# Performance work log

Hardware: AMD Instinct MI355X
Metric: run time of the kernel (lower is better)

Reference implementation:

```python
import jax, jax.numpy as jnp
import numpy as np

D, B, L, E, H, F = 6, 4, 2048, 1024, 16, 4096
DH = E // H
DECAY = 16.0
CSCALE = 1.0
EPS = 1e-5


def _ln(x, w, b):
    m = jnp.mean(x, axis=-1, keepdims=True)
    v = jnp.mean(jnp.square(x - m), axis=-1, keepdims=True)
    return (x - m) * jax.lax.rsqrt(v + EPS) * w + b


def setup_inputs() -> dict:
    key = jax.random.key(0)
    ks = jax.random.split(key, 10)
    s = 0.02
    f32 = jnp.float32
    return {
        "x": jax.random.normal(ks[0], (B, L, E), f32),
        "Wq": jax.random.normal(ks[1], (D, E, E), f32) * s,
        "Wk": jax.random.normal(ks[2], (D, E, E), f32) * s,
        "bq": jnp.zeros((D, E), f32),
        "bk": jnp.zeros((D, E), f32),
        "ln1_w": jnp.ones((D, E), f32), "ln1_b": jnp.zeros((D, E), f32),
        "ln2_w": jnp.ones((D, E), f32), "ln2_b": jnp.zeros((D, E), f32),
        "ln3_w": jnp.ones((D, E), f32), "ln3_b": jnp.zeros((D, E), f32),
        "W1": jax.random.normal(ks[3], (D, F, E), f32) * s,
        "b1": jnp.zeros((D, F), f32),
        "W2": jax.random.normal(ks[4], (D, E, F), f32) * s,
        "b2": jnp.zeros((D, E), f32),
    }


def reference(x, Wq, Wk, bq, bk, ln1_w, ln1_b, ln2_w, ln2_b, ln3_w, ln3_b, W1, b1, W2, b2):
    seq = x.shape[1]
    pos = jnp.arange(seq)
    # exponential relative-position bias exp(-|i-j|/decay), shared by all layers
    rel = jnp.exp(-jnp.abs(pos[:, None] - pos[None, :]).astype(x.dtype) / DECAY)
    inv_sqrt_d = 1.0 / np.sqrt(DH)

    def layer(h, p):
        (wq, wk, bq_, bk_, l1w, l1b, l2w, l2b, l3w, l3b, w1, b1_, w2, b2_) = p
        bh, sl, _ = h.shape
        q = (h @ wq.T + bq_).reshape(bh, sl, H, DH)
        k = (h @ wk.T + bk_).reshape(bh, sl, H, DH)
        scores = jnp.einsum('blhd,bmhd->bhlm', q, k) * inv_sqrt_d
        # torch MHA need_weights=True averages softmax weights over heads
        w_avg = jax.nn.softmax(scores, axis=-1).mean(axis=1)  # [B,L,L]
        new_w = jax.nn.softmax(CSCALE * w_avg + rel[None], axis=-1)
        sa = jnp.einsum('blm,bme->ble', new_w, h)  # value = raw residual stream
        h1 = _ln(h + sa, l1w, l1b)
        h2 = _ln(h1, l2w, l2b)  # Noop cross-attn block (LayerNorm scale-invariant)
        ff = jax.nn.relu(h2 @ w1.T + b1_) @ w2.T + b2_
        return _ln(h2 + ff, l3w, l3b), None

    out, _ = jax.lax.scan(layer, x, (Wq, Wk, bq, bk, ln1_w, ln1_b, ln2_w, ln2_b,
                                     ln3_w, ln3_b, W1, b1, W2, b2))
    return out
```

## Files before the change

### kernel.cpp

```cpp
#include <hip/hip_runtime.h>

#define D_ 6
#define B_ 4
#define L_ 2048
#define E_ 1024
#define H_ 16
#define F_ 4096
#define BL_ (B_ * L_)
#define QKS 2048
#define EPS_ 1e-5f
#define EXPSC 0.18033688011112042f
#define LOG2E 1.4426950408889634f
#define LOG2E_H (LOG2E / 16.0f)

typedef __bf16 bf16x8 __attribute__((ext_vector_type(8)));
typedef __bf16 bf16x4 __attribute__((ext_vector_type(4)));
typedef float f32x4 __attribute__((ext_vector_type(4)));

__device__ __forceinline__ float fexp2(float x) {
  return __builtin_amdgcn_exp2f(x);
}

__device__ __forceinline__ void gload_lds16(const void* g, void* l) {
  __builtin_amdgcn_global_load_lds(
      (const __attribute__((address_space(1))) void*)g,
      (__attribute__((address_space(3))) void*)l, 16, 0, 0);
}

__device__ __forceinline__ void stage_tile64(__bf16* ldsb,
                                             const __bf16* gbase, long ldg,
                                             int tid) {
#pragma unroll
  for (int j = 0; j < 2; ++j) {
    int unit = j * 256 + tid;
    int row = unit >> 3, cu = unit & 7;
    const __bf16* src = gbase + (long)row * ldg + ((cu ^ (row & 7)) << 3);
    gload_lds16(src, ldsb + (long)((j * 256 + (tid & ~63)) << 3));
  }
}

#define RD_FRAG(ldsb, r_, kk) \
  (*(const bf16x8*)&(ldsb)[((r_) * 8 + (((kk) * 4 + l4) ^ ((r_) & 7))) * 8])

#define LDA_SUB(P, MH)                                                        \
  _Pragma("unroll") for (int mi = 0; mi < 4; ++mi)                            \
  _Pragma("unroll") for (int kk = 0; kk < 2; ++kk) {                          \
    int r_ = wr + (MH) * 64 + mi * 16 + l15;                                  \
    int cu_ = kk * 4 + l4;                                                    \
    aF[mi][kk] = *(const bf16x8*)&lds[P][0][(r_ * 8 + (cu_ ^ (r_ & 7))) * 8]; \
  }

#define LDB_SUB(P, BF, NH)                                                    \
  _Pragma("unroll") for (int ni = 0; ni < 2; ++ni)                            \
  _Pragma("unroll") for (int kk = 0; kk < 2; ++kk) {                          \
    int r_ = wc + (NH) * 32 + ni * 16 + l15;                                  \
    int cu_ = kk * 4 + l4;                                                    \
    BF[ni][kk] = *(const bf16x8*)&lds[P][1][(r_ * 8 + (cu_ ^ (r_ & 7))) * 8]; \
  }

#define MFMA_Q(AF, BF, MH, NH)                                                \
  _Pragma("unroll") for (int mi = 0; mi < 4; ++mi)                            \
  _Pragma("unroll") for (int ni = 0; ni < 2; ++ni)                            \
  _Pragma("unroll") for (int kk = 0; kk < 2; ++kk)                            \
    acc[(MH) * 4 + mi][(NH) * 2 + ni] =                                       \
        __builtin_amdgcn_mfma_f32_16x16x32_bf16(                              \
            AF[mi][kk], BF[ni][kk], acc[(MH) * 4 + mi][(NH) * 2 + ni], 0, 0, 0);

#define PHASE_PRE()                                                           \
  __builtin_amdgcn_s_barrier();                                               \
  asm volatile("s_waitcnt lgkmcnt(0)" ::: "memory");                          \
  __builtin_amdgcn_sched_barrier(0);                                          \
  __builtin_amdgcn_s_setprio(1)

#define PHASE_POST()                                                          \
  __builtin_amdgcn_s_setprio(0);                                              \
  __builtin_amdgcn_sched_barrier(0);                                          \
  __builtin_amdgcn_s_barrier()

#define STAGE_A(BUFI, HF, K0)                                                 \
  do {                                                                        \
    gload_lds16(sA[HF][0] + (K0),                                             \
                &lds[BUFI][0][((HF) * 1024 + wave * 64) * 8]);                \
    gload_lds16(sA[HF][1] + (K0),                                             \
                &lds[BUFI][0][((HF) * 1024 + 512 + wave * 64) * 8]);          \
  } while (0)

#define STAGE_B(BUFI, HF, K0)                                                 \
  do {                                                                        \
    gload_lds16(sB[HF][0] + (K0),                                             \
                &lds[BUFI][1][((HF) * 1024 + wave * 64) * 8]);                \
    gload_lds16(sB[HF][1] + (K0),                                             \
                &lds[BUFI][1][((HF) * 1024 + 512 + wave * 64) * 8]);          \
  } while (0)

template <int EPI>
__global__ __launch_bounds__(512, 2) void gemm8p(
    const __bf16* __restrict__ A, const __bf16* __restrict__ Bm,
    __bf16* __restrict__ Cb, const float* __restrict__ bias, int M, int N,
    int K, int lda, int ldb, int zk, long strA, long strB, long strC,
    long strCk) {
  __shared__ __bf16 lds[2][2][256 * 64];
  const int tid = threadIdx.x;
  const int wave = tid >> 6, lane = tid & 63;
  const int l15 = lane & 15, l4 = lane >> 4;
  const int z = blockIdx.y;
  const int kc = (zk == 2) ? (z & 1) : 0;
  const int bat = (zk == 2) ? (z >> 1) : z;
  const __bf16* Ab = A + (long)bat * strA + (long)kc * K;
  const __bf16* Bb = Bm + (long)bat * strB + (long)kc * K;
  const long coff = (long)bat * strC + (long)kc * strCk;

  const int nbx = N >> 8;
  const int nwg = (M >> 8) * nbx;
  const int orig = blockIdx.x;
  const int qq = nwg >> 3, rr = nwg & 7;
  const int xcd = orig & 7, lid = orig >> 3;
  const int wg = (xcd < rr ? xcd * (qq + 1) : rr * (qq + 1) + (xcd - rr) * qq) + lid;
  const int row0 = (wg / nbx) * 256, col0 = (wg % nbx) * 256;
  const int wr = (wave >> 2) * 128;
  const int wc = (wave & 3) * 64;

  const int rsel = tid >> 3;
  const int swz = ((lane & 7) ^ (rsel & 7)) << 3;
  const __bf16* sA[2][2];
  const __bf16* sB[2][2];
#pragma unroll
  for (int hf = 0; hf < 2; ++hf)
#pragma unroll
    for (int j = 0; j < 2; ++j) {
      sA[hf][j] = Ab + (long)(row0 + hf * 128 + j * 64 + rsel) * lda + swz;
      sB[hf][j] = Bb + (long)(col0 + hf * 128 + j * 64 + rsel) * ldb + swz;
    }

  const int NT = K >> 6;
  STAGE_A(0, 0, 0);
  STAGE_A(0, 1, 0);
  STAGE_B(0, 0, 0);
  STAGE_B(0, 1, 0);
  STAGE_A(1, 0, 64);
  STAGE_B(1, 0, 64);
  STAGE_A(1, 1, 64);
  asm volatile("s_waitcnt vmcnt(6)" ::: "memory");
  __builtin_amdgcn_s_barrier();

  f32x4 acc[8][4];
#pragma unroll
  for (int i = 0; i < 8; ++i)
#pragma unroll
    for (int j = 0; j < 4; ++j) acc[i][j] = (f32x4){0.f, 0.f, 0.f, 0.f};
  bf16x8 aF[4][2], b0F[2][2], b1F[2][2];

  for (int t = 0; t < NT; ++t) {
    const int p = t & 1;
    const int kA = (t + 1 < NT ? t + 1 : NT - 1) << 6;
    const int kB = (t + 2 < NT ? t + 2 : NT - 1) << 6;
    LDA_SUB(p, 0);
    LDB_SUB(p, b0F, 0);
    STAGE_B(p ^ 1, 1, kA);
    PHASE_PRE();
    MFMA_Q(aF, b0F, 0, 0);
    PHASE_POST();
    LDB_SUB(p, b1F, 1);
    PHASE_PRE();
    MFMA_Q(aF, b1F, 0, 1);
    PHASE_POST();
    LDA_SUB(p, 1);
    STAGE_B(p, 0, kB);
    PHASE_PRE();
    MFMA_Q(aF, b0F, 1, 0);
    PHASE_POST();
    STAGE_A(p, 0, kB);
    STAGE_A(p, 1, kB);
    __builtin_amdgcn_s_barrier();
    __builtin_amdgcn_sched_barrier(0);
    __builtin_amdgcn_s_setprio(1);
    MFMA_Q(aF, b1F, 1, 1);
    __builtin_amdgcn_s_setprio(0);
    __builtin_amdgcn_sched_barrier(0);
    asm volatile("s_waitcnt vmcnt(6)" ::: "memory");
    __builtin_amdgcn_s_barrier();
  }
  asm volatile("s_waitcnt vmcnt(0)" ::: "memory");

#pragma unroll
  for (int i = 0; i < 8; ++i) {
    int row = row0 + wr + (i >> 2) * 64 + (i & 3) * 16 + l4 * 4;
#pragma unroll
    for (int j = 0; j < 4; ++j) {
      int col = col0 + wc + (j >> 1) * 32 + (j & 1) * 16 + l15;
      float bval = 0.f;
      if constexpr (EPI == 1 || EPI == 2) bval = bias[col];
#pragma unroll
      for (int r = 0; r < 4; ++r) {
        long crow = row + r;
        float v = acc[i][j][r];
        if constexpr (EPI == 1 || EPI == 2) v += bval;
        if constexpr (EPI == 2) v = fmaxf(v, 0.f);
        Cb[coff + crow * N + col] = (__bf16)v;
      }
    }
  }
}

__global__ __launch_bounds__(256, 4) void attn_stats_kernel(
    const __bf16* __restrict__ qk, float* __restrict__ sinv) {
  __shared__ __bf16 sQ[64 * 64];
  __shared__ __bf16 sK[2][64 * 64];
  const int tid = threadIdx.x, wave = tid >> 6, lane = tid & 63;
  const int l15 = lane & 15, l4 = lane >> 4;
  const int l0 = blockIdx.x * 64, h = blockIdx.y, b = blockIdx.z;
  const __bf16* Qb = qk + ((long)(b * L_ + l0)) * QKS + h * 64;
  const __bf16* Kb = qk + ((long)b * L_) * QKS + 1024 + h * 64;

  stage_tile64(sQ, Qb, QKS, tid);
  stage_tile64(sK[0], Kb, QKS, tid);
  asm volatile("s_waitcnt vmcnt(0)" ::: "memory");
  __builtin_amdgcn_s_barrier();

  const int rA = wave * 16 + l15;
  const bf16x8 aF0 = RD_FRAG(sQ, rA, 0);
  const bf16x8 aF1 = RD_FRAG(sQ, rA, 1);

  float msum[4] = {0.f, 0.f, 0.f, 0.f};
  int p = 0;
  for (int m0 = 0; m0 < 32; ++m0) {
    const int mn = (m0 + 1 < 32) ? m0 + 1 : 31;
    stage_tile64(sK[p ^ 1], Kb + (long)mn * 64 * QKS, QKS, tid);
    asm volatile("s_waitcnt vmcnt(2)" ::: "memory");
    __builtin_amdgcn_s_barrier();
#pragma unroll
    for (int ni = 0; ni < 4; ++ni) {
      const int rB = ni * 16 + l15;
      bf16x8 b0 = RD_FRAG(sK[p], rB, 0);
      bf16x8 b1 = RD_FRAG(sK[p], rB, 1);
      f32x4 s = (f32x4){0.f, 0.f, 0.f, 0.f};
      s = __builtin_amdgcn_mfma_f32_16x16x32_bf16(aF0, b0, s, 0, 0, 0);
      s = __builtin_amdgcn_mfma_f32_16x16x32_bf16(aF1, b1, s, 0, 0, 0);
#pragma unroll
      for (int r = 0; r < 4; ++r) msum[r] += fexp2(s[r]);
    }
    asm volatile("" ::: "memory");
    __builtin_amdgcn_s_barrier();
    p ^= 1;
  }
#pragma unroll
  for (int r = 0; r < 4; ++r) {
    float s = msum[r];
    for (int d = 1; d < 16; d <<= 1) s += __shfl_xor(s, d, 64);
    msum[r] = s;
  }
  if (l15 == 0) {
    long idx = ((long)(b * H_ + h)) * L_ + l0 + wave * 16 + l4 * 4;
    f32x4 o = {1.0f / msum[0], 1.0f / msum[1], 1.0f / msum[2], 1.0f / msum[3]};
    *(f32x4*)&sinv[idx] = o;
  }
}

__global__ __launch_bounds__(256, 4) void attn_probs_kernel(
    const __bf16* __restrict__ qk, const float* __restrict__ sinv,
    const float* __restrict__ relTab, __bf16* __restrict__ P,
    float* __restrict__ rowsumT) {
  __shared__ __bf16 sT[2][2][64 * 64];
  const int tid = threadIdx.x, wave = tid >> 6, lane = tid & 63;
  const int l15 = lane & 15, l4 = lane >> 4;
  const int m0 = blockIdx.x * 64, l0 = blockIdx.y * 64, b = blockIdx.z;
  const __bf16* Qb = qk + ((long)(b * L_ + l0)) * QKS;
  const __bf16* Kb = qk + ((long)(b * L_ + m0)) * QKS + 1024;

  stage_tile64(sT[0][0], Qb, QKS, tid);
  stage_tile64(sT[0][1], Kb, QKS, tid);

  float wacc[4][4];
#pragma unroll
  for (int i = 0; i < 4; ++i)
#pragma unroll
    for (int j = 0; j < 4; ++j) wacc[i][j] = 0.f;

  const int rA = wave * 16 + l15;
  const int row0 = l0 + wave * 16 + l4 * 4;
  int p = 0;
  for (int h = 0; h < H_; ++h) {
    const int hn = (h + 1 < H_) ? h + 1 : H_ - 1;
    stage_tile64(sT[p ^ 1][0], Qb + hn * 64, QKS, tid);
    stage_tile64(sT[p ^ 1][1], Kb + hn * 64, QKS, tid);
    f32x4 iv = *(const f32x4*)&sinv[((long)(b * H_ + h)) * L_ + row0];
    asm volatile("s_waitcnt vmcnt(4)" ::: "memory");
    __builtin_amdgcn_s_barrier();
    bf16x8 aF0 = RD_FRAG(sT[p][0], rA, 0);
    bf16x8 aF1 = RD_FRAG(sT[p][0], rA, 1);
#pragma unroll
    for (int ni = 0; ni < 4; ++ni) {
      const int rB = ni * 16 + l15;
      bf16x8 b0 = RD_FRAG(sT[p][1], rB, 0);
      bf16x8 b1 = RD_FRAG(sT[p][1], rB, 1);
      f32x4 s = (f32x4){0.f, 0.f, 0.f, 0.f};
      s = __builtin_amdgcn_mfma_f32_16x16x32_bf16(aF0, b0, s, 0, 0, 0);
      s = __builtin_amdgcn_mfma_f32_16x16x32_bf16(aF1, b1, s, 0, 0, 0);
#pragma unroll
      for (int r = 0; r < 4; ++r) wacc[ni][r] += fexp2(s[r]) * iv[r];
    }
    asm volatile("" ::: "memory");
    __builtin_amdgcn_s_barrier();
    p ^= 1;
  }
  float rowpart[4] = {0.f, 0.f, 0.f, 0.f};
#pragma unroll
  for (int ni = 0; ni < 4; ++ni) {
#pragma unroll
    for (int r = 0; r < 4; ++r) {
      int row = row0 + r;
      int col = m0 + ni * 16 + l15;
      float relL = relTab[row - col + 2048];
      float pv = fexp2(fmaf(wacc[ni][r], LOG2E_H, relL));
      P[((long)b * L_ + row) * L_ + col] = (__bf16)pv;
      rowpart[r] += pv;
    }
  }
#pragma unroll
  for (int r = 0; r < 4; ++r) {
    float s = rowpart[r];
    s += __shfl_xor(s, 1, 16);
    s += __shfl_xor(s, 2, 16);
    s += __shfl_xor(s, 4, 16);
    s += __shfl_xor(s, 8, 16);
    if (l15 == 0)
      rowsumT[((long)b * L_ + row0 + r) * 32 + (m0 >> 6)] = s;
  }
}

__device__ __forceinline__ void wave_reduce2(float& a, float& b) {
#pragma unroll
  for (int d = 1; d < 64; d <<= 1) {
    a += __shfl_xor(a, d, 64);
    b += __shfl_xor(b, d, 64);
  }
}

__global__ __launch_bounds__(256, 4) void ln12_kernel(
    const float* __restrict__ hin, const __bf16* __restrict__ p0,
    const __bf16* __restrict__ p1, const float* __restrict__ rowsumT,
    const float* __restrict__ w1, const float* __restrict__ b1,
    const float* __restrict__ w2, const float* __restrict__ b2,
    float* __restrict__ h2f, __bf16* __restrict__ h2b) {
  __shared__ float sh[9];
  const int tid = threadIdx.x;
  const long row = blockIdx.x;
  const long base = row * E_ + tid * 4;
  if (tid < 32) {
    float s = rowsumT[row * 32 + tid];
#pragma unroll
    for (int d = 1; d < 32; d <<= 1) s += __shfl_xor(s, d, 32);
    if (tid == 0) sh[8] = s;
  }
  f32x4 hv = *(const f32x4*)&hin[base];
  bf16x4 p0v = *(const bf16x4*)&p0[base];
  bf16x4 p1v = *(const bf16x4*)&p1[base];
  __syncthreads();
  const float rinv = 1.0f / sh[8];
  float y[4];
  float s1 = 0.f, s2 = 0.f;
#pragma unroll
  for (int j = 0; j < 4; ++j) {
    y[j] = hv[j] + rinv * ((float)p0v[j] + (float)p1v[j]);
    s1 += y[j];
    s2 += y[j] * y[j];
  }
  wave_reduce2(s1, s2);
  if ((tid & 63) == 0) { sh[(tid >> 6) * 2] = s1; sh[(tid >> 6) * 2 + 1] = s2; }
  __syncthreads();
  s1 = sh[0] + sh[2] + sh[4] + sh[6];
  s2 = sh[1] + sh[3] + sh[5] + sh[7];
  float mean = s1 * (1.f / E_);
  float var = s2 * (1.f / E_) - mean * mean;
  float rs = rsqrtf(var + EPS_);
  f32x4 wv = *(const f32x4*)&w1[tid * 4];
  f32x4 bv = *(const f32x4*)&b1[tid * 4];
  float h1[4];
  s1 = 0.f; s2 = 0.f;
#pragma unroll
  for (int j = 0; j < 4; ++j) {
    h1[j] = (y[j] - mean) * rs * wv[j] + bv[j];
    s1 += h1[j];
    s2 += h1[j] * h1[j];
  }
  __syncthreads();
  wave_reduce2(s1, s2);
  if ((tid & 63) == 0) { sh[(tid >> 6) * 2] = s1; sh[(tid >> 6) * 2 + 1] = s2; }
  __syncthreads();
  s1 = sh[0] + sh[2] + sh[4] + sh[6];
  s2 = sh[1] + sh[3] + sh[5] + sh[7];
  mean = s1 * (1.f / E_);
  var = s2 * (1.f / E_) - mean * mean;
  rs = rsqrtf(var + EPS_);
  wv = *(const f32x4*)&w2[tid * 4];
  bv = *(const f32x4*)&b2[tid * 4];
  f32x4 o;
  bf16x4 ob;
#pragma unroll
  for (int j = 0; j < 4; ++j) {
    float v = (h1[j] - mean) * rs * wv[j] + bv[j];
    o[j] = v;
    ob[j] = (__bf16)v;
  }
  *(f32x4*)&h2f[base] = o;
  *(bf16x4*)&h2b[base] = ob;
}

__global__ __launch_bounds__(256, 4) void ln3_kernel(
    const float* __restrict__ h2f, const __bf16* __restrict__ p0,
    const __bf16* __restrict__ p1, const float* __restrict__ bias2,
    const float* __restrict__ w3, const float* __restrict__ b3,
    float* __restrict__ outf, __bf16* __restrict__ outb) {
  __shared__ float sh[8];
  const int tid = threadIdx.x;
  const long row = blockIdx.x;
  const long base = row * E_ + tid * 4;
  f32x4 hv = *(const f32x4*)&h2f[base];
  bf16x4 p0v = *(const bf16x4*)&p0[base];
  bf16x4 p1v = *(const bf16x4*)&p1[base];
  f32x4 b2v = *(const f32x4*)&bias2[tid * 4];
  float y[4];
  float s1 = 0.f, s2 = 0.f;
#pragma unroll
  for (int j = 0; j < 4; ++j) {
    y[j] = hv[j] + (float)p0v[j] + (float)p1v[j] + b2v[j];
    s1 += y[j];
    s2 += y[j] * y[j];
  }
  wave_reduce2(s1, s2);
  if ((tid & 63) == 0) { sh[(tid >> 6) * 2] = s1; sh[(tid >> 6) * 2 + 1] = s2; }
  __syncthreads();
  s1 = sh[0] + sh[2] + sh[4] + sh[6];
  s2 = sh[1] + sh[3] + sh[5] + sh[7];
  float mean = s1 * (1.f / E_);
  float var = s2 * (1.f / E_) - mean * mean;
  float rs = rsqrtf(var + EPS_);
  f32x4 wv = *(const f32x4*)&w3[tid * 4];
  f32x4 bv = *(const f32x4*)&b3[tid * 4];
  f32x4 o;
  bf16x4 ob;
#pragma unroll
  for (int j = 0; j < 4; ++j) {
    float v = (y[j] - mean) * rs * wv[j] + bv[j];
    o[j] = v;
    ob[j] = (__bf16)v;
  }
  *(f32x4*)&outf[base] = o;
  *(bf16x4*)&outb[base] = ob;
}

__global__ __launch_bounds__(256, 4) void transpose_kernel(
    const __bf16* __restrict__ X, __bf16* __restrict__ XT) {
  __shared__ __bf16 t[64 * 66];
  const int l0 = blockIdx.x * 64, e0 = blockIdx.y * 64, b = blockIdx.z;
  const int tid = threadIdx.x;
#pragma unroll
  for (int r = 0; r < 2; ++r) {
    int c = tid + 256 * r;
    int rw = c >> 3, c8 = (c & 7) * 8;
    *(bf16x8*)&t[rw * 66 + c8] =
        *(const bf16x8*)&X[((long)(b * L_) + l0 + rw) * E_ + e0 + c8];
  }
  __syncthreads();
#pragma unroll
  for (int r = 0; r < 2; ++r) {
    int c = tid + 256 * r;
    int er = c >> 3, l8 = (c & 7) * 8;
    bf16x8 v;
#pragma unroll
    for (int j = 0; j < 8; ++j) v[j] = t[(l8 + j) * 66 + er];
    *(bf16x8*)&XT[((long)(b * E_) + e0 + er) * L_ + l0 + l8] = v;
  }
}

__global__ __launch_bounds__(256, 4) void f32_to_bf16_kernel(
    const float* __restrict__ x, __bf16* __restrict__ y) {
  long i = ((long)blockIdx.x * 256 + threadIdx.x) * 4;
  f32x4 v = *(const f32x4*)&x[i];
  bf16x4 o;
#pragma unroll
  for (int j = 0; j < 4; ++j) o[j] = (__bf16)v[j];
  *(bf16x4*)&y[i] = o;
}

__global__ __launch_bounds__(256, 4) void build_wqk_kernel(
    const float* __restrict__ Wq, const float* __restrict__ Wk,
    __bf16* __restrict__ out) {
  long i = ((long)blockIdx.x * 256 + threadIdx.x) * 4;
  long d = i >> 21;
  long rem = i & ((1L << 21) - 1);
  long row = rem >> 10, col = rem & 1023;
  const bool isQ = (row < 1024);
  const float* src = isQ ? &Wq[(d << 20) + (row << 10) + col]
                         : &Wk[(d << 20) + ((row - 1024) << 10) + col];
  const float sc = isQ ? EXPSC : 1.0f;
  f32x4 v = *(const f32x4*)src;
  bf16x4 o;
#pragma unroll
  for (int j = 0; j < 4; ++j) o[j] = (__bf16)(v[j] * sc);
  *(bf16x4*)&out[i] = o;
}

__global__ __launch_bounds__(256, 4) void build_bqk_kernel(
    const float* __restrict__ bq, const float* __restrict__ bk,
    float* __restrict__ out) {
  int i = blockIdx.x * 256 + threadIdx.x;
  int d = i >> 11, c = i & 2047;
  out[i] = (c < 1024) ? bq[d * 1024 + c] * EXPSC : bk[d * 1024 + c - 1024];
}

__global__ __launch_bounds__(256, 4) void build_rel_kernel(
    float* __restrict__ relTab) {
  int i = blockIdx.x * 256 + threadIdx.x;
  relTab[i] = __expf(-fabsf((float)(i - 2048)) * (1.0f / 16.0f)) * LOG2E;
}

extern "C" void kernel_launch(void* const* d_in, const int* in_sizes, int n_in,
                              void* d_out, int out_size, void* d_ws,
                              size_t ws_size, hipStream_t stream) {
  const float* x = (const float*)d_in[0];
  const float* Wq = (const float*)d_in[1];
  const float* Wk = (const float*)d_in[2];
  const float* bq = (const float*)d_in[3];
  const float* bk = (const float*)d_in[4];
  const float* l1w = (const float*)d_in[5];
  const float* l1b = (const float*)d_in[6];
  const float* l2w = (const float*)d_in[7];
  const float* l2b = (const float*)d_in[8];
  const float* l3w = (const float*)d_in[9];
  const float* l3b = (const float*)d_in[10];
  const float* W1 = (const float*)d_in[11];
  const float* b1 = (const float*)d_in[12];
  const float* W2 = (const float*)d_in[13];
  const float* b2 = (const float*)d_in[14];

  char* p = (char*)d_ws;
  auto take = [&](size_t bytes) -> char* {
    char* r = p;
    p += (bytes + 255) & ~(size_t)255;
    return r;
  };
  __bf16* wqk_bf = (__bf16*)take((size_t)D_ * 2048 * 1024 * 2);
  __bf16* w1_bf = (__bf16*)take((size_t)D_ * F_ * E_ * 2);
  __bf16* w2_bf = (__bf16*)take((size_t)D_ * E_ * F_ * 2);
  __bf16* h_bf = (__bf16*)take((size_t)BL_ * E_ * 2);
  __bf16* hT = (__bf16*)take((size_t)BL_ * E_ * 2);
  __bf16* qk_bf = (__bf16*)take((size_t)BL_ * QKS * 2);
  __bf16* Pbuf = (__bf16*)take((size_t)B_ * L_ * L_ * 2);
  __bf16* ffmid = qk_bf;
  float* bqk = (float*)take((size_t)D_ * 2048 * 4);
  float* relTab = (float*)take((size_t)4096 * 4);
  float* sinv = (float*)take((size_t)B_ * H_ * L_ * 4);
  float* rowsumT = (float*)take((size_t)BL_ * 32 * 4);
  __bf16* partB = (__bf16*)take((size_t)2 * BL_ * E_ * 2);
  __bf16* part0 = partB;
  __bf16* part1 = partB + (size_t)BL_ * E_;
  float* hbuf = (float*)take((size_t)BL_ * E_ * 4);

  build_wqk_kernel<<<D_ * 2048 * 1024 / 1024, 256, 0, stream>>>(Wq, Wk, wqk_bf);
  build_bqk_kernel<<<D_ * 2048 / 256, 256, 0, stream>>>(bq, bk, bqk);
  build_rel_kernel<<<16, 256, 0, stream>>>(relTab);
  f32_to_bf16_kernel<<<D_ * F_ * E_ / 1024, 256, 0, stream>>>(W1, w1_bf);
  f32_to_bf16_kernel<<<D_ * E_ * F_ / 1024, 256, 0, stream>>>(W2, w2_bf);
  f32_to_bf16_kernel<<<BL_ * E_ / 1024, 256, 0, stream>>>(x, h_bf);
  transpose_kernel<<<dim3(L_ / 64, E_ / 64, B_), 256, 0, stream>>>(h_bf, hT);

  const float* h_in = x;
  for (int d = 0; d < D_; ++d) {
    gemm8p<1><<<dim3(256, 1), 512, 0, stream>>>(
        h_bf, wqk_bf + (size_t)d * 2048 * 1024, qk_bf, bqk + d * 2048, BL_,
        2048, E_, E_, E_, 1, 0, 0, 0, 0);
    attn_stats_kernel<<<dim3(L_ / 64, H_, B_), 256, 0, stream>>>(qk_bf, sinv);
    attn_probs_kernel<<<dim3(L_ / 64, L_ / 64, B_), 256, 0, stream>>>(
        qk_bf, sinv, relTab, Pbuf, rowsumT);
    gemm8p<0><<<dim3(32, 8), 512, 0, stream>>>(
        Pbuf, hT, partB, nullptr, L_, E_, L_ / 2, L_, L_, 2, (long)L_ * L_,
        (long)E_ * L_, (long)L_ * E_, (long)BL_ * E_);
    ln12_kernel<<<BL_, 256, 0, stream>>>(h_in, part0, part1, rowsumT,
                                         l1w + d * E_, l1b + d * E_,
                                         l2w + d * E_, l2b + d * E_, hbuf,
                                         h_bf);
    gemm8p<2><<<dim3(512, 1), 512, 0, stream>>>(
        h_bf, w1_bf + (size_t)d * F_ * E_, ffmid, b1 + d * F_, BL_, F_, E_,
        E_, E_, 1, 0, 0, 0, 0);
    gemm8p<0><<<dim3(128, 2), 512, 0, stream>>>(
        ffmid, w2_bf + (size_t)d * E_ * F_, partB, nullptr, BL_, E_, F_ / 2,
        F_, F_, 2, 0, 0, 0, (long)BL_ * E_);
    float* outp = (d == D_ - 1) ? (float*)d_out : hbuf;
    ln3_kernel<<<BL_, 256, 0, stream>>>(hbuf, part0, part1, b2 + d * E_,
                                        l3w + d * E_, l3b + d * E_, outp,
                                        h_bf);
    if (d < D_ - 1) {
      transpose_kernel<<<dim3(L_ / 64, E_ / 64, B_), 256, 0, stream>>>(h_bf, hT);
      h_in = hbuf;
    }
  }
}
```

Before: 2.325 ms.

## Enlarge attention stats/probs tiles to 128 rows with 512-thread blocks

The attention statistics kernel now processes 128 query rows per block with 8 waves, so each staged K tile is reused by twice as many rows. The probabilities kernel moves from 64x64 to 128x128 output tiles with 8 waves, each computing 32x64, which cuts redundant global/LDS loads of Q and K per head. The cost is more LDS and registers per block, lower occupancy (launch bounds 2) and fewer blocks in the grid.

```diff
diff --git a/kernel.cpp b/kernel.cpp
--- a/kernel.cpp
+++ b/kernel.cpp
@@ -36,6 +36,26 @@
     int row = unit >> 3, cu = unit & 7;
     const __bf16* src = gbase + (long)row * ldg + ((cu ^ (row & 7)) << 3);
     gload_lds16(src, ldsb + (long)((j * 256 + (tid & ~63)) << 3));
+  }
+}
+
+__device__ __forceinline__ void stage_tile64_512(__bf16* ldsb,
+                                                 const __bf16* gbase, long ldg,
+                                                 int tid) {
+  int row = tid >> 3, cu = tid & 7;
+  const __bf16* src = gbase + (long)row * ldg + ((cu ^ (row & 7)) << 3);
+  gload_lds16(src, ldsb + (long)((tid & ~63) << 3));
+}
+
+__device__ __forceinline__ void stage_tile128_512(__bf16* ldsb,
+                                                  const __bf16* gbase,
+                                                  long ldg, int tid) {
+#pragma unroll
+  for (int j = 0; j < 2; ++j) {
+    int unit = j * 512 + tid;
+    int row = unit >> 3, cu = unit & 7;
+    const __bf16* src = gbase + (long)row * ldg + ((cu ^ (row & 7)) << 3);
+    gload_lds16(src, ldsb + (long)((j * 512 + (tid & ~63)) << 3));
   }
 }
 
@@ -202,18 +222,18 @@
   }
 }
 
-__global__ __launch_bounds__(256, 4) void attn_stats_kernel(
+__global__ __launch_bounds__(512, 4) void attn_stats_kernel(
     const __bf16* __restrict__ qk, float* __restrict__ sinv) {
-  __shared__ __bf16 sQ[64 * 64];
+  __shared__ __bf16 sQ[128 * 64];
   __shared__ __bf16 sK[2][64 * 64];
   const int tid = threadIdx.x, wave = tid >> 6, lane = tid & 63;
   const int l15 = lane & 15, l4 = lane >> 4;
-  const int l0 = blockIdx.x * 64, h = blockIdx.y, b = blockIdx.z;
+  const int l0 = blockIdx.x * 128, h = blockIdx.y, b = blockIdx.z;
   const __bf16* Qb = qk + ((long)(b * L_ + l0)) * QKS + h * 64;
   const __bf16* Kb = qk + ((long)b * L_) * QKS + 1024 + h * 64;
 
-  stage_tile64(sQ, Qb, QKS, tid);
-  stage_tile64(sK[0], Kb, QKS, tid);
+  stage_tile128_512(sQ, Qb, QKS, tid);
+  stage_tile64_512(sK[0], Kb, QKS, tid);
   asm volatile("s_waitcnt vmcnt(0)" ::: "memory");
   __builtin_amdgcn_s_barrier();
 
@@ -225,8 +245,8 @@
   int p = 0;
   for (int m0 = 0; m0 < 32; ++m0) {
     const int mn = (m0 + 1 < 32) ? m0 + 1 : 31;
-    stage_tile64(sK[p ^ 1], Kb + (long)mn * 64 * QKS, QKS, tid);
-    asm volatile("s_waitcnt vmcnt(2)" ::: "memory");
+    stage_tile64_512(sK[p ^ 1], Kb + (long)mn * 64 * QKS, QKS, tid);
+    asm volatile("s_waitcnt vmcnt(1)" ::: "memory");
     __builtin_amdgcn_s_barrier();
 #pragma unroll
     for (int ni = 0; ni < 4; ++ni) {
@@ -256,75 +276,94 @@
   }
 }
 
-__global__ __launch_bounds__(256, 4) void attn_probs_kernel(
+__global__ __launch_bounds__(512, 2) void attn_probs_kernel(
     const __bf16* __restrict__ qk, const float* __restrict__ sinv,
     const float* __restrict__ relTab, __bf16* __restrict__ P,
     float* __restrict__ rowsumT) {
-  __shared__ __bf16 sT[2][2][64 * 64];
+  __shared__ __bf16 sQ[2][128 * 64];
+  __shared__ __bf16 sKl[2][128 * 64];
   const int tid = threadIdx.x, wave = tid >> 6, lane = tid & 63;
   const int l15 = lane & 15, l4 = lane >> 4;
-  const int m0 = blockIdx.x * 64, l0 = blockIdx.y * 64, b = blockIdx.z;
+  const int m0 = blockIdx.x * 128, l0 = blockIdx.y * 128, b = blockIdx.z;
+  const int wr2 = wave & 3, wc2 = wave >> 2;
   const __bf16* Qb = qk + ((long)(b * L_ + l0)) * QKS;
   const __bf16* Kb = qk + ((long)(b * L_ + m0)) * QKS + 1024;
 
-  stage_tile64(sT[0][0], Qb, QKS, tid);
-  stage_tile64(sT[0][1], Kb, QKS, tid);
-
-  float wacc[4][4];
+  stage_tile128_512(sQ[0], Qb, QKS, tid);
+  stage_tile128_512(sKl[0], Kb, QKS, tid);
+
+  float wacc[4][8];
 #pragma unroll
   for (int i = 0; i < 4; ++i)
 #pragma unroll
-    for (int j = 0; j < 4; ++j) wacc[i][j] = 0.f;
-
-  const int rA = wave * 16 + l15;
-  const int row0 = l0 + wave * 16 + l4 * 4;
+    for (int j = 0; j < 8; ++j) wacc[i][j] = 0.f;
+
+  const int rA0 = wr2 * 32 + l15;
+  const int rowbase = l0 + wr2 * 32 + l4 * 4;
   int p = 0;
   for (int h = 0; h < H_; ++h) {
     const int hn = (h + 1 < H_) ? h + 1 : H_ - 1;
-    stage_tile64(sT[p ^ 1][0], Qb + hn * 64, QKS, tid);
-    stage_tile64(sT[p ^ 1][1], Kb + hn * 64, QKS, tid);
-    f32x4 iv = *(const f32x4*)&sinv[((long)(b * H_ + h)) * L_ + row0];
+    stage_tile128_512(sQ[p ^ 1], Qb + hn * 64, QKS, tid);
+    stage_tile128_512(sKl[p ^ 1], Kb + hn * 64, QKS, tid);
+    const float* svh = &sinv[((long)(b * H_ + h)) * L_];
+    f32x4 iv0 = *(const f32x4*)&svh[rowbase];
+    f32x4 iv1 = *(const f32x4*)&svh[rowbase + 16];
     asm volatile("s_waitcnt vmcnt(4)" ::: "memory");
     __builtin_amdgcn_s_barrier();
-    bf16x8 aF0 = RD_FRAG(sT[p][0], rA, 0);
-    bf16x8 aF1 = RD_FRAG(sT[p][0], rA, 1);
+    bf16x8 aF[2][2];
+    aF[0][0] = RD_FRAG(sQ[p], rA0, 0);
+    aF[0][1] = RD_FRAG(sQ[p], rA0, 1);
+    aF[1][0] = RD_FRAG(sQ[p], rA0 + 16, 0);
+    aF[1][1] = RD_FRAG(sQ[p], rA0 + 16, 1);
 #pragma unroll
     for (int ni = 0; ni < 4; ++ni) {
-      const int rB = ni * 16 + l15;
-      bf16x8 b0 = RD_FRAG(sT[p][1], rB, 0);
-      bf16x8 b1 = RD_FRAG(sT[p][1], rB, 1);
-      f32x4 s = (f32x4){0.f, 0.f, 0.f, 0.f};
-      s = __builtin_amdgcn_mfma_f32_16x16x32_bf16(aF0, b0, s, 0, 0, 0);
-      s = __builtin_amdgcn_mfma_f32_16x16x32_bf16(aF1, b1, s, 0, 0, 0);
-#pragma unroll
-      for (int r = 0; r < 4; ++r) wacc[ni][r] += fexp2(s[r]) * iv[r];
+      const int rB = wc2 * 64 + ni * 16 + l15;
+      bf16x8 b0 = RD_FRAG(sKl[p], rB, 0);
+      bf16x8 b1 = RD_FRAG(sKl[p], rB, 1);
+#pragma unroll
+      for (int fi = 0; fi < 2; ++fi) {
+        f32x4 s = (f32x4){0.f, 0.f, 0.f, 0.f};
+        s = __builtin_amdgcn_mfma_f32_16x16x32_bf16(aF[fi][0], b0, s, 0, 0, 0);
+        s = __builtin_amdgcn_mfma_f32_16x16x32_bf16(aF[fi][1], b1, s, 0, 0, 0);
+#pragma unroll
+        for (int r = 0; r < 4; ++r)
+          wacc[ni][fi * 4 + r] += fexp2(s[r]) * (fi ? iv1[r] : iv0[r]);
+      }
     }
     asm volatile("" ::: "memory");
     __builtin_amdgcn_s_barrier();
     p ^= 1;
   }
-  float rowpart[4] = {0.f, 0.f, 0.f, 0.f};
+  float rowpart[2][4] = {{0.f, 0.f, 0.f, 0.f}, {0.f, 0.f, 0.f, 0.f}};
 #pragma unroll
   for (int ni = 0; ni < 4; ++ni) {
 #pragma unroll
+    for (int fi = 0; fi < 2; ++fi) {
+#pragma unroll
+      for (int r = 0; r < 4; ++r) {
+        int row = rowbase + fi * 16 + r;
+        int col = m0 + wc2 * 64 + ni * 16 + l15;
+        float relL = relTab[row - col + 2048];
+        float pv = fexp2(fmaf(wacc[ni][fi * 4 + r], LOG2E_H, relL));
+        P[((long)b * L_ + row) * L_ + col] = (__bf16)pv;
+        rowpart[fi][r] += pv;
+      }
+    }
+  }
+#pragma unroll
+  for (int fi = 0; fi < 2; ++fi) {
+#pragma unroll
     for (int r = 0; r < 4; ++r) {
-      int row = row0 + r;
-      int col = m0 + ni * 16 + l15;
-      float relL = relTab[row - col + 2048];
-      float pv = fexp2(fmaf(wacc[ni][r], LOG2E_H, relL));
-      P[((long)b * L_ + row) * L_ + col] = (__bf16)pv;
-      rowpart[r] += pv;
+      float s = rowpart[fi][r];
+      s += __shfl_xor(s, 1, 16);
+      s += __shfl_xor(s, 2, 16);
+      s += __shfl_xor(s, 4, 16);
+      s += __shfl_xor(s, 8, 16);
+      if (l15 == 0) {
+        int row = rowbase + fi * 16 + r;
+        rowsumT[((long)b * L_ + row) * 32 + (m0 >> 6) + wc2] = s;
+      }
     }
-  }
-#pragma unroll
-  for (int r = 0; r < 4; ++r) {
-    float s = rowpart[r];
-    s += __shfl_xor(s, 1, 16);
-    s += __shfl_xor(s, 2, 16);
-    s += __shfl_xor(s, 4, 16);
-    s += __shfl_xor(s, 8, 16);
-    if (l15 == 0)
-      rowsumT[((long)b * L_ + row0 + r) * 32 + (m0 >> 6)] = s;
   }
 }
 
@@ -570,8 +609,8 @@
     gemm8p<1><<<dim3(256, 1), 512, 0, stream>>>(
         h_bf, wqk_bf + (size_t)d * 2048 * 1024, qk_bf, bqk + d * 2048, BL_,
         2048, E_, E_, E_, 1, 0, 0, 0, 0);
-    attn_stats_kernel<<<dim3(L_ / 64, H_, B_), 256, 0, stream>>>(qk_bf, sinv);
-    attn_probs_kernel<<<dim3(L_ / 64, L_ / 64, B_), 256, 0, stream>>>(
+    attn_stats_kernel<<<dim3(L_ / 128, H_, B_), 512, 0, stream>>>(qk_bf, sinv);
+    attn_probs_kernel<<<dim3(L_ / 128, L_ / 128, B_), 512, 0, stream>>>(
         qk_bf, sinv, relTab, Pbuf, rowsumT);
     gemm8p<0><<<dim3(32, 8), 512, 0, stream>>>(
         Pbuf, hT, partB, nullptr, L_, E_, L_ / 2, L_, L_, 2, (long)L_ * L_,
```

Measured after the change: 2.253 ms. -3.1%, faster.
